# Kernel optimization log

Hardware: AMD Instinct MI355X
Metric: run time of the kernel (lower is better)

## Reference

```python
import jax, jax.numpy as jnp
import numpy as np

B, S, T, V, E, H, D, A = 16, 128, 128, 32000, 512, 512, 512, 512
ENC = 2 * H  # bidirectional encoder output dim
NEG = -1e9


def _w(key, shape, scale=0.05):
    return scale * jax.random.normal(key, shape, dtype=jnp.float32)


def setup_inputs() -> dict:
    key = jax.random.key(0)
    ks = jax.random.split(key, 26)
    src = jax.random.randint(ks[0], (B, S), 1, V)
    tgt = jax.random.randint(ks[1], (B, T), 1, V)
    src_lens = jnp.full((B,), S, dtype=jnp.int32)  # full-length sequences (pack == identity)
    return dict(
        src=src, src_lens=src_lens, tgt=tgt,
        enc_embed=_w(ks[2], (V, E)).at[0].set(0.0),   # padding_idx=0
        Wih_f=_w(ks[3], (4 * H, E)), Whh_f=_w(ks[4], (4 * H, H)),
        bih_f=_w(ks[5], (4 * H,)), bhh_f=_w(ks[6], (4 * H,)),
        Wih_b=_w(ks[7], (4 * H, E)), Whh_b=_w(ks[8], (4 * H, H)),
        bih_b=_w(ks[9], (4 * H,)), bhh_b=_w(ks[10], (4 * H,)),
        Wbh=_w(ks[11], (D, 2 * H)), bbh=_w(ks[12], (D,)),
        Wbc=_w(ks[13], (D, 2 * H)), bbc=_w(ks[14], (D,)),
        Wh_att=_w(ks[15], (A, ENC)), Ws_att=_w(ks[16], (A, D)), v_att=_w(ks[17], (A,)),
        dec_embed=_w(ks[18], (V, E)).at[0].set(0.0),  # padding_idx=0
        Wih_d=_w(ks[19], (4 * D, E + ENC)), Whh_d=_w(ks[20], (4 * D, D)),
        bih_d=_w(ks[21], (4 * D,)), bhh_d=_w(ks[22], (4 * D,)),
        Wfc=_w(ks[23], (V, D + ENC)), bfc=_w(ks[24], (V,)),
    )


def _lstm_cell(x, h, c, Wih, Whh, bih, bhh):
    # PyTorch gate order: i, f, g, o
    g = x @ Wih.T + h @ Whh.T + (bih + bhh)
    i, f, gg, o = jnp.split(g, 4, axis=-1)
    c = jax.nn.sigmoid(f) * c + jax.nn.sigmoid(i) * jnp.tanh(gg)
    h = jax.nn.sigmoid(o) * jnp.tanh(c)
    return h, c


def _run_lstm(xs, Wih, Whh, bih, bhh, hdim):
    # xs: [S, B, E] -> (hs [S, B, hdim], h_last, c_last)
    b = xs.shape[1]
    h0 = jnp.zeros((b, hdim), xs.dtype)

    def step(carry, x):
        h, c = carry
        h, c = _lstm_cell(x, h, c, Wih, Whh, bih, bhh)
        return (h, c), h

    (hT, cT), hs = jax.lax.scan(step, (h0, h0), xs)
    return hs, hT, cT


def reference(src, src_lens, tgt, enc_embed, Wih_f, Whh_f, bih_f, bhh_f,
              Wih_b, Whh_b, bih_b, bhh_b, Wbh, bbh, Wbc, bbc,
              Wh_att, Ws_att, v_att, dec_embed, Wih_d, Whh_d, bih_d, bhh_d,
              Wfc, bfc):
    # ---- BiLSTM encoder (src_lens == S, so packing is the identity) ----
    emb = enc_embed[src]                      # [B, S, E]
    xs = jnp.swapaxes(emb, 0, 1)              # [S, B, E]
    hs_f, hf, _ = _run_lstm(xs, Wih_f, Whh_f, bih_f, bhh_f, H)
    hs_b, hb, _ = _run_lstm(xs[::-1], Wih_b, Whh_b, bih_b, bhh_b, H)
    hs_b = hs_b[::-1]
    enc_out = jnp.swapaxes(jnp.concatenate([hs_f, hs_b], axis=-1), 0, 1)  # [B, S, 2H]

    # ---- bridge (num_layers = 1) ----
    h_cat = jnp.concatenate([hf, hb], axis=-1)  # [B, 2H]
    h0 = jnp.tanh(h_cat @ Wbh.T + bbh)          # [B, D]
    c_cat = jnp.concatenate([hf, hb], axis=-1)
    c0 = jnp.tanh(c_cat @ Wbc.T + bbc)

    mask = jnp.arange(S)[None, :] < src_lens[:, None]  # [B, S]
    enc_proj = jnp.einsum('bse,ae->bsa', enc_out, Wh_att)  # W_h(enc_out), hoisted

    # ---- decoder loop, teacher_forcing = 1.0 ----
    def dec_step(carry, inp_t):
        h, c = carry
        # Bahdanau attention on top-layer hidden state
        score = jnp.einsum('bsa,a->bs', jnp.tanh(enc_proj + (h @ Ws_att.T)[:, None, :]), v_att)
        score = jnp.where(mask, score, NEG)
        attn = jax.nn.softmax(score, axis=-1)
        ctx = jnp.einsum('bs,bse->be', attn, enc_out)       # [B, 2H]
        x = jnp.concatenate([dec_embed[inp_t], ctx], axis=-1)  # [B, E+2H]
        h, c = _lstm_cell(x, h, c, Wih_d, Whh_d, bih_d, bhh_d)
        logits = jnp.concatenate([h, ctx], axis=-1) @ Wfc.T + bfc  # [B, V]
        return (h, c), logits

    inps = tgt[:, :-1].T  # [T-1, B]
    _, logits = jax.lax.scan(dec_step, (h0, c0), inps)
    return jnp.swapaxes(logits, 0, 1)  # [B, T-1, V]
```

## Files before the change

kernel.cpp:

```cpp
#include <hip/hip_runtime.h>

typedef __bf16 bf16x8 __attribute__((ext_vector_type(8)));
typedef float f32x4 __attribute__((ext_vector_type(4)));
typedef unsigned short us;
typedef unsigned long long ull;

#define DEV static __device__ __forceinline__

DEV float bf2f(us u){ union { unsigned u; float f; } x; x.u = ((unsigned)u) << 16; return x.f; }
DEV us f2bf(float f){
  union { float f; unsigned u; } x; x.f = f;
  unsigned r = x.u + 0x7fffu + ((x.u >> 16) & 1u);
  return (us)(r >> 16);
}
DEV unsigned pack2(us lo, us hi){ return (unsigned)lo | ((unsigned)hi << 16); }
DEV float sigm(float x){ return 1.0f / (1.0f + expf(-x)); }
DEV float tanh_fast(float x){ float e = __expf(2.0f * x); return 1.0f - 2.0f / (e + 1.0f); }
DEV void unpk2(unsigned u, float& a, float& b){ a = bf2f((us)u); b = bf2f((us)(u >> 16)); }

DEV unsigned ld4v(const unsigned* p){ return __hip_atomic_load(p, __ATOMIC_RELAXED, __HIP_MEMORY_SCOPE_AGENT); }
DEV ull ld8v(const void* p){ return __hip_atomic_load((const ull*)p, __ATOMIC_RELAXED, __HIP_MEMORY_SCOPE_AGENT); }
DEV void st4v(unsigned* p, unsigned v){ __hip_atomic_store(p, v, __ATOMIC_RELAXED, __HIP_MEMORY_SCOPE_AGENT); }

DEV void gridbar3(unsigned* arr, unsigned ep){
  __syncthreads();
  if (threadIdx.x == 0)
    __hip_atomic_store(arr + (size_t)blockIdx.x * 16, ep, __ATOMIC_RELEASE, __HIP_MEMORY_SCOPE_AGENT);
  if (threadIdx.x < 128){
    while (__hip_atomic_load(arr + (size_t)threadIdx.x * 16, __ATOMIC_RELAXED, __HIP_MEMORY_SCOPE_AGENT) < ep)
      __builtin_amdgcn_s_sleep(4);
  }
  __syncthreads();
}

DEV void groupbar(unsigned* gbase, int slot, unsigned ep){
  __syncthreads();
  if (threadIdx.x == 0)
    __hip_atomic_store(gbase + slot * 16, ep, __ATOMIC_RELEASE, __HIP_MEMORY_SCOPE_AGENT);
  if (threadIdx.x < 8){
    while (__hip_atomic_load(gbase + threadIdx.x * 16, __ATOMIC_RELAXED, __HIP_MEMORY_SCOPE_AGENT) < ep)
      __builtin_amdgcn_s_sleep(2);
  }
  __syncthreads();
}

__global__ void k_f2bf(const float4* __restrict__ in, uint2* __restrict__ out, long n4){
  long stride = (long)gridDim.x * blockDim.x;
  for (long i = (long)blockIdx.x * blockDim.x + threadIdx.x; i < n4; i += stride){
    float4 v = in[i];
    uint2 o; o.x = pack2(f2bf(v.x), f2bf(v.y)); o.y = pack2(f2bf(v.z), f2bf(v.w));
    out[i] = o;
  }
}

__global__ void k_bias3(const float* a0, const float* b0, float* o0,
                        const float* a1, const float* b1, float* o1,
                        const float* a2, const float* b2, float* o2){
  int i = blockIdx.x * 256 + threadIdx.x;
  o0[i] = a0[i] + b0[i];
  o1[i] = a1[i] + b1[i];
  o2[i] = a2[i] + b2[i];
}

__global__ void k_embed(const int* __restrict__ tok, const float* __restrict__ table,
                        us* __restrict__ out){
  int r = blockIdx.x;
  int b = r & 15, pos = r >> 4;
  int idx = tok[b * 128 + pos];
  float4 v = ((const float4*)(table + (size_t)idx * 512))[threadIdx.x];
  uint2 o; o.x = pack2(f2bf(v.x), f2bf(v.y)); o.y = pack2(f2bf(v.z), f2bf(v.w));
  ((uint2*)(out + (size_t)r * 512))[threadIdx.x] = o;
}

template<int MODE>
__global__ __launch_bounds__(256)
void gemm_bt(const us* __restrict__ A, int lda,
             const us* __restrict__ B, int ldb,
             const float* __restrict__ bias,
             void* __restrict__ Cv, int ldc, int K, int mvalid)
{
  __shared__ __align__(16) us As[128 * 64];
  __shared__ __align__(16) us Bs[128 * 64];
  const int tid  = threadIdx.x;
  const int lane = tid & 63, wid = tid >> 6;
  const int wm = (wid >> 1) * 64, wn = (wid & 1) * 64;
  const us* Ab = A + (size_t)blockIdx.y * 128 * lda;
  const us* Bb = B + (size_t)blockIdx.x * 128 * ldb;

  f32x4 acc[4][4] = {};
  bf16x8 ga[4], gb[4];

  #pragma unroll
  for (int r = 0; r < 4; r++){
    int c = tid + r * 256;
    ga[r] = *(const bf16x8*)(Ab + (size_t)(c >> 3) * lda + (c & 7) * 8);
    gb[r] = *(const bf16x8*)(Bb + (size_t)(c >> 3) * ldb + (c & 7) * 8);
  }
  const int nt = K >> 6;
  for (int t = 0; t < nt; t++){
    #pragma unroll
    for (int r = 0; r < 4; r++){
      int c = tid + r * 256;
      int slot = ((c >> 3) * 8 + ((c & 7) ^ ((c >> 3) & 7))) * 8;
      *(bf16x8*)(As + slot) = ga[r];
      *(bf16x8*)(Bs + slot) = gb[r];
    }
    __syncthreads();
    if (t + 1 < nt){
      int k0 = (t + 1) * 64;
      #pragma unroll
      for (int r = 0; r < 4; r++){
        int c = tid + r * 256;
        ga[r] = *(const bf16x8*)(Ab + (size_t)(c >> 3) * lda + k0 + (c & 7) * 8);
        gb[r] = *(const bf16x8*)(Bb + (size_t)(c >> 3) * ldb + k0 + (c & 7) * 8);
      }
    }
    #pragma unroll
    for (int kk = 0; kk < 2; kk++){
      bf16x8 av[4], bv[4];
      #pragma unroll
      for (int i = 0; i < 4; i++){
        int ra = wm + i * 16 + (lane & 15);
        int ua = (kk * 4 + (lane >> 4)) ^ (ra & 7);
        av[i] = *(const bf16x8*)(As + (ra * 8 + ua) * 8);
        int rb = wn + i * 16 + (lane & 15);
        int ub = (kk * 4 + (lane >> 4)) ^ (rb & 7);
        bv[i] = *(const bf16x8*)(Bs + (rb * 8 + ub) * 8);
      }
      #pragma unroll
      for (int i = 0; i < 4; i++)
        #pragma unroll
        for (int j = 0; j < 4; j++)
          acc[i][j] = __builtin_amdgcn_mfma_f32_16x16x32_bf16(av[i], bv[j], acc[i][j], 0, 0, 0);
    }
    if (t + 1 < nt) __syncthreads();
  }

  const int cb = lane & 15, rb4 = (lane >> 4) * 4;
  #pragma unroll
  for (int i = 0; i < 4; i++){
    #pragma unroll
    for (int j = 0; j < 4; j++){
      #pragma unroll
      for (int r = 0; r < 4; r++){
        int row = blockIdx.y * 128 + wm + i * 16 + rb4 + r;
        int col = blockIdx.x * 128 + wn + j * 16 + cb;
        float v = acc[i][j][r];
        if (bias) v += bias[col];
        if (MODE == 0) ((float*)Cv)[(size_t)row * ldc + col] = v;
        else           ((us*)Cv)[(size_t)row * ldc + col] = f2bf(v);
      }
    }
  }
}

__global__ __launch_bounds__(256)
void enc_persist4(const float* __restrict__ gin_f, const float* __restrict__ gin_b,
                  const us* __restrict__ whhf_bf, const us* __restrict__ whhb_bf,
                  us* __restrict__ enc_out_bf,
                  unsigned* __restrict__ arr)
{
  __shared__ __align__(16) us Wt[2][1024][8];
  __shared__ __align__(16) us Hrow[2][16][520];
  __shared__ __align__(16) f32x4 P[2][4][64];
  __shared__ float gl[2][16][17];
  __shared__ float hvout[2][16][4];

  const int bx = blockIdx.x, tid = threadIdx.x;
  const int lane = tid & 63, wv = tid >> 6;

  for (int d = 0; d < 2; d++){
    const us* srcw = d ? whhb_bf : whhf_bf;
    for (int u = tid; u < 1024; u += 256){
      int ks = u >> 6, ch = (u >> 4) & 3, v = u & 15;
      int n = (v & 3) * 512 + bx * 4 + (v >> 2);
      *(bf16x8*)Wt[d][u] = *(const bf16x8*)(srcw + (size_t)n * 512 + ks * 32 + ch * 8);
    }
  }

  float creg = 0.0f;
  const int cd = (tid >> 6) & 1, cb = tid & 15, cj = (tid >> 4) & 3;

  for (int t = 0; t < 128; t++){
    if (t == 0){
      #pragma unroll
      for (int r = 0; r < 8; r++){
        int u = tid + r * 256;
        int d = u >> 10, b = (u >> 6) & 15, s16 = u & 63;
        *(ull*)&Hrow[d][b][s16 * 8]     = 0ull;
        *(ull*)&Hrow[d][b][s16 * 8 + 4] = 0ull;
      }
    } else {
      #pragma unroll
      for (int r = 0; r < 8; r++){
        int u = tid + r * 256;
        int d = u >> 10, b = (u >> 6) & 15, s16 = u & 63;
        int sp = d ? (128 - t) : (t - 1);
        const us* s = enc_out_bf + ((size_t)b * 128 + sp) * 1024 + d * 512 + s16 * 8;
        ull lo = ld8v(s), hi = ld8v(s + 4);
        *(ull*)&Hrow[d][b][s16 * 8]     = lo;
        *(ull*)&Hrow[d][b][s16 * 8 + 4] = hi;
      }
    }
    __syncthreads();
    #pragma unroll
    for (int d = 0; d < 2; d++){
      f32x4 acc = {};
      #pragma unroll
      for (int m = 0; m < 4; m++){
        int ks = wv * 4 + m;
        int ch = lane >> 4, b = lane & 15;
        acc = __builtin_amdgcn_mfma_f32_16x16x32_bf16(*(const bf16x8*)&Hrow[d][b][ks * 32 + ch * 8],
                                                      *(const bf16x8*)Wt[d][(ks * 4 + ch) * 16 + b],
                                                      acc, 0, 0, 0);
      }
      P[d][wv][lane] = acc;
    }
    __syncthreads();
    if (wv < 2){
      int d = wv;
      f32x4 sum = (P[d][0][lane] + P[d][1][lane]) + (P[d][2][lane] + P[d][3][lane]);
      int v = lane & 15;
      int n = (v & 3) * 512 + bx * 4 + (v >> 2);
      int s_in = d ? (127 - t) : t;
      const float* gg = (d ? gin_b : gin_f) + (size_t)s_in * 16 * 2048 + n;
      #pragma unroll
      for (int r = 0; r < 4; r++){
        int b = (lane >> 4) * 4 + r;
        gl[d][v][b] = sum[r] + gg[(size_t)b * 2048];
      }
    }
    __syncthreads();
    if (tid < 128){
      float ig = sigm (gl[cd][cj * 4 + 0][cb]);
      float fg = sigm (gl[cd][cj * 4 + 1][cb]);
      float g2 = tanhf(gl[cd][cj * 4 + 2][cb]);
      float og = sigm (gl[cd][cj * 4 + 3][cb]);
      float cn = fg * creg + ig * g2;
      float hv = og * tanhf(cn);
      creg = cn;
      hvout[cd][cb][cj] = hv;
    }
    __syncthreads();
    if (tid < 64){
      int d = tid >> 5, rem = tid & 31, b = rem & 15, jp = rem >> 4;
      int s_in = d ? (127 - t) : t;
      st4v((unsigned*)(enc_out_bf + ((size_t)b * 128 + s_in) * 1024 + d * 512 + bx * 4 + jp * 2),
           pack2(f2bf(hvout[d][b][jp * 2]), f2bf(hvout[d][b][jp * 2 + 1])));
    }
    if (t != 127) gridbar3(arr, t + 1);
  }
}

__global__ __launch_bounds__(512)
void k_h0c0(const us* __restrict__ enc_out_bf, const float* __restrict__ Wbh, const float* __restrict__ bbh,
            const float* __restrict__ Wbc, const float* __restrict__ bbc,
            us* __restrict__ h0_bf, float* __restrict__ c_dec)
{
  __shared__ float hc[1024];
  int b = blockIdx.x >> 1, which = blockIdx.x & 1;
  int tid = threadIdx.x;
  hc[tid]       = bf2f(enc_out_bf[((size_t)b * 128 + 127) * 1024 + tid]);
  hc[512 + tid] = bf2f(enc_out_bf[((size_t)b * 128 + 0)   * 1024 + 512 + tid]);
  __syncthreads();
  const float* W = which ? Wbc : Wbh;
  float acc = (which ? bbc : bbh)[tid];
  const float* wr = W + (size_t)tid * 1024;
  for (int k = 0; k < 1024; k += 4){
    float4 w = *(const float4*)(wr + k);
    acc += w.x * hc[k] + w.y * hc[k + 1] + w.z * hc[k + 2] + w.w * hc[k + 3];
  }
  float v = tanhf(acc);
  if (which) c_dec[b * 512 + tid] = v;
  else       h0_bf[b * 512 + tid] = f2bf(v);
}

#define SMEM_BYTES 161952

__global__ __launch_bounds__(256)
void dec_fused2(const us* __restrict__ h0_bf, const float* __restrict__ c_dec0,
                const float* __restrict__ Ws_att, const float* __restrict__ v_att,
                const us* __restrict__ enc_proj_bf, const us* __restrict__ enc_out_bf,
                const int* __restrict__ src_lens, const float* __restrict__ gin_d,
                const us* __restrict__ whhd_bf, const us* __restrict__ wihd_bf,
                float* __restrict__ hs_g, float* __restrict__ esc_g,
                us* __restrict__ hctx,
                const us* __restrict__ wfc, const float* __restrict__ bfc,
                float* __restrict__ out,
                unsigned* __restrict__ arr, unsigned* __restrict__ arrG,
                unsigned* __restrict__ tdone)
{
  __shared__ __align__(16) char smem[SMEM_BYTES];
  const int tid = threadIdx.x;

  if (blockIdx.x >= 128){
    us* As = (us*)smem;
    us* Bs = (us*)(smem + 32768);
    const int lane = tid & 63, wid = tid >> 6;
    const int wm = wid * 64;
    for (int tile = blockIdx.x - 128; tile < 2000; tile += 128){
      int rt = tile / 250, ct = tile - rt * 250;
      unsigned need = (rt == 7) ? 127u : (unsigned)(16 * rt + 16);
      if (tid == 0){
        while (ld4v(tdone) < need) __builtin_amdgcn_s_sleep(8);
      }
      __syncthreads();
      const us* Ab = hctx + (size_t)rt * 256 * 1536;
      const us* Bb = wfc  + (size_t)ct * 128 * 1536;
      f32x4 acc[4][8] = {};
      bf16x8 ga[8], gb[4];
      #pragma unroll
      for (int r = 0; r < 8; r++){
        int cc = tid + r * 256;
        int row = cc >> 3, piece = cc & 7;
        bool val = (rt * 256 + row) < 2032;
        union { ull q[2]; bf16x8 v; } u;
        const us* p = Ab + (size_t)row * 1536 + piece * 8;
        u.q[0] = val ? ld8v(p) : 0ull;
        u.q[1] = val ? ld8v(p + 4) : 0ull;
        ga[r] = u.v;
      }
      #pragma unroll
      for (int r = 0; r < 4; r++){
        int cc = tid + r * 256;
        gb[r] = *(const bf16x8*)(Bb + (size_t)(cc >> 3) * 1536 + (cc & 7) * 8);
      }
      for (int tk = 0; tk < 24; tk++){
        #pragma unroll
        for (int r = 0; r < 8; r++){
          int cc = tid + r * 256;
          int slot = ((cc >> 3) * 8 + ((cc & 7) ^ ((cc >> 3) & 7))) * 8;
          *(bf16x8*)(As + slot) = ga[r];
        }
        #pragma unroll
        for (int r = 0; r < 4; r++){
          int cc = tid + r * 256;
          int slot = ((cc >> 3) * 8 + ((cc & 7) ^ ((cc >> 3) & 7))) * 8;
          *(bf16x8*)(Bs + slot) = gb[r];
        }
        __syncthreads();
        if (tk + 1 < 24){
          int k0 = (tk + 1) * 64;
          #pragma unroll
          for (int r = 0; r < 8; r++){
            int cc = tid + r * 256;
            int row = cc >> 3, piece = cc & 7;
            bool val = (rt * 256 + row) < 2032;
            union { ull q[2]; bf16x8 v; } u;
            const us* p = Ab + (size_t)row * 1536 + k0 + piece * 8;
            u.q[0] = val ? ld8v(p) : 0ull;
            u.q[1] = val ? ld8v(p + 4) : 0ull;
            ga[r] = u.v;
          }
          #pragma unroll
          for (int r = 0; r < 4; r++){
            int cc = tid + r * 256;
            gb[r] = *(const bf16x8*)(Bb + (size_t)(cc >> 3) * 1536 + k0 + (cc & 7) * 8);
          }
        }
        #pragma unroll
        for (int kk = 0; kk < 2; kk++){
          bf16x8 av[4], bv[8];
          #pragma unroll
          for (int i = 0; i < 4; i++){
            int ra = wm + i * 16 + (lane & 15);
            int ua = (kk * 4 + (lane >> 4)) ^ (ra & 7);
            av[i] = *(const bf16x8*)(As + (ra * 8 + ua) * 8);
          }
          #pragma unroll
          for (int j = 0; j < 8; j++){
            int rb = j * 16 + (lane & 15);
            int ub = (kk * 4 + (lane >> 4)) ^ (rb & 7);
            bv[j] = *(const bf16x8*)(Bs + (rb * 8 + ub) * 8);
          }
          #pragma unroll
          for (int i = 0; i < 4; i++)
            #pragma unroll
            for (int j = 0; j < 8; j++)
              acc[i][j] = __builtin_amdgcn_mfma_f32_16x16x32_bf16(av[i], bv[j], acc[i][j], 0, 0, 0);
        }
        if (tk + 1 < 24) __syncthreads();
      }
      const int cbl = lane & 15, rb4 = (lane >> 4) * 4;
      #pragma unroll
      for (int i = 0; i < 4; i++){
        #pragma unroll
        for (int j = 0; j < 8; j++){
          #pragma unroll
          for (int r = 0; r < 4; r++){
            int row = rt * 256 + wm + i * 16 + rb4 + r;
            int col = ct * 128 + j * 16 + cbl;
            if (row < 2032){
              float v = acc[i][j][r] + bfc[col];
              int tt = row >> 4, b = row & 15;
              out[((size_t)b * 127 + tt) * 32000 + col] = v;
            }
          }
        }
      }
    }
    return;
  }

  us (*Wh)[8]      = (us(*)[8])(smem);
  us (*Wc)[8]      = (us(*)[8])(smem + 16384);
  us (*Ws64)[520]  = (us(*)[520])(smem + 49152);
  us (*Xrow)[1032] = (us(*)[1032])(smem + 115712);
  f32x4 (*P)[64]   = (f32x4(*)[64])(smem + 148736);
  float (*g1l)[17] = (float(*)[17])(smem + 152832);
  float (*gl)[17]  = (float(*)[17])(smem + 153920);
  float* vl        = (float*)(smem + 155008);
  float (*hsp)[64] = (float(*)[64])(smem + 157056);
  float* hs_b      = (float*)(smem + 158080);
  float* att       = (float*)(smem + 160128);
  float (*cred)[128] = (float(*)[128])(smem + 160640);
  float* sred      = (float*)(smem + 161664);
  float (*hvs)[4]  = (float(*)[4])(smem + 161696);

  const int bx = blockIdx.x;
  const int lane = tid & 63, wv = tid >> 6;
  const int bB = bx & 15, sQ = bx >> 4;
  unsigned* gbase = arrG + bB * 128;

  for (int u = tid; u < 1024; u += 256){
    int ks = u >> 6, ch = (u >> 4) & 3, v = u & 15;
    int n = (v & 3) * 512 + bx * 4 + (v >> 2);
    *(bf16x8*)Wh[u] = *(const bf16x8*)(whhd_bf + (size_t)n * 512 + ks * 32 + ch * 8);
  }
  for (int u = tid; u < 2048; u += 256){
    int ks = u >> 6, ch = (u >> 4) & 3, v = u & 15;
    int n = (v & 3) * 512 + bx * 4 + (v >> 2);
    *(bf16x8*)Wc[u] = *(const bf16x8*)(wihd_bf + (size_t)n * 1536 + 512 + ks * 32 + ch * 8);
  }
  for (int u = tid; u < 32768; u += 256){
    int a = u >> 9, k = u & 511;
    Ws64[a][k] = f2bf(Ws_att[(size_t)(sQ * 64 + a) * 512 + k]);
  }
  for (int u = tid; u < 512; u += 256) vl[u] = v_att[u];
  const int slen = src_lens[bB];

  float creg = 0.0f;
  if (tid < 64) creg = c_dec0[(tid & 15) * 512 + bx * 4 + (tid >> 4)];

  for (int t = 0; t < 127; t++){
    const us* hsrc = t ? (hctx + (size_t)(t - 1) * 16 * 1536) : h0_bf;
    const int hstride = t ? 1536 : 512;

    #pragma unroll
    for (int r = 0; r < 4; r++){
      int u = tid + r * 256;
      int b = u >> 6, s16 = u & 63;
      const us* s = hsrc + (size_t)b * hstride + s16 * 8;
      ull lo = ld8v(s), hi = ld8v(s + 4);
      *(ull*)&Xrow[b][s16 * 8]     = lo;
      *(ull*)&Xrow[b][s16 * 8 + 4] = hi;
    }
    __syncthreads();
    {
      f32x4 acc = {};
      #pragma unroll
      for (int m = 0; m < 4; m++){
        int ks = wv * 4 + m;
        int ch = lane >> 4, b = lane & 15;
        acc = __builtin_amdgcn_mfma_f32_16x16x32_bf16(*(const bf16x8*)&Xrow[b][ks * 32 + ch * 8],
                                                      *(const bf16x8*)Wh[(ks * 4 + ch) * 16 + b],
                                                      acc, 0, 0, 0);
      }
      P[wv][lane] = acc;
    }
    {
      const us* wr = Ws64[lane] + wv * 128;
      const us* xr = Xrow[bB] + wv * 128;
      float s = 0.f;
      #pragma unroll
      for (int k = 0; k < 128; k += 8){
        bf16x8 xv = *(const bf16x8*)(xr + k);
        bf16x8 wv8 = *(const bf16x8*)(wr + k);
        #pragma unroll
        for (int e = 0; e < 8; e++) s += (float)xv[e] * (float)wv8[e];
      }
      hsp[wv][lane] = s;
    }
    __syncthreads();
    if (wv == 0){
      f32x4 sum = (P[0][lane] + P[1][lane]) + (P[2][lane] + P[3][lane]);
      int v = lane & 15;
      int n = (v & 3) * 512 + bx * 4 + (v >> 2);
      #pragma unroll
      for (int r = 0; r < 4; r++){
        int b = (lane >> 4) * 4 + r;
        g1l[v][b] = sum[r] + gin_d[((size_t)t * 16 + b) * 2048 + n];
      }
    }
    if (tid < 64){
      float v = hsp[0][tid] + hsp[1][tid] + hsp[2][tid] + hsp[3][tid];
      st4v((unsigned*)&hs_g[bB * 512 + sQ * 64 + tid], __float_as_uint(v));
    }

    groupbar(gbase, sQ, 2 * t + 1);

    {
      ull v = ld8v(&hs_g[bB * 512 + tid * 2]);
      *(ull*)&hs_b[tid * 2] = v;
    }
    __syncthreads();
    {
      int si = tid >> 4, part = tid & 15;
      const us* er = enc_proj_bf + ((size_t)bB * 128 + sQ * 16 + si) * 512 + part * 32;
      const float* hb = hs_b + part * 32;
      const float* vp = vl + part * 32;
      float sv = 0.f;
      #pragma unroll
      for (int a = 0; a < 32; a += 8){
        uint4 u4 = *(const uint4*)(er + a);
        float e0,e1,e2,e3,e4,e5,e6,e7;
        unpk2(u4.x,e0,e1); unpk2(u4.y,e2,e3); unpk2(u4.z,e4,e5); unpk2(u4.w,e6,e7);
        sv += vp[a+0]*tanh_fast(e0+hb[a+0]) + vp[a+1]*tanh_fast(e1+hb[a+1])
            + vp[a+2]*tanh_fast(e2+hb[a+2]) + vp[a+3]*tanh_fast(e3+hb[a+3])
            + vp[a+4]*tanh_fast(e4+hb[a+4]) + vp[a+5]*tanh_fast(e5+hb[a+5])
            + vp[a+6]*tanh_fast(e6+hb[a+6]) + vp[a+7]*tanh_fast(e7+hb[a+7]);
      }
      sv += __shfl_xor(sv, 1);
      sv += __shfl_xor(sv, 2);
      sv += __shfl_xor(sv, 4);
      sv += __shfl_xor(sv, 8);
      if (part == 0){
        int s = sQ * 16 + si;
        float e = (s < slen) ? __expf(sv) : 0.f;
        st4v((unsigned*)&esc_g[bB * 128 + s], __float_as_uint(e));
      }
    }

    groupbar(gbase, sQ, 2 * t + 2);

    {
      float e = 0.f;
      if (tid < 128) e = __uint_as_float(ld4v((unsigned*)&esc_g[bB * 128 + tid]));
      if (tid < 128) att[tid] = e;
      float ss = e;
      #pragma unroll
      for (int o = 32; o; o >>= 1) ss += __shfl_xor(ss, o);
      if (lane == 0) sred[wv] = ss;
    }
    __syncthreads();
    {
      int kk = tid & 127, half = tid >> 7;
      const float* ab = att + half * 64;
      const us* er = enc_out_bf + ((size_t)(bB * 128 + half * 64)) * 1024 + sQ * 128 + kk;
      float s = 0.f;
      #pragma unroll 8
      for (int s2 = 0; s2 < 64; s2++)
        s += ab[s2] * bf2f(er[(size_t)s2 * 1024]);
      cred[half][kk] = s;
    }
    __syncthreads();
    if (tid < 64){
      float inv = 1.0f / (sred[0] + sred[1] + sred[2] + sred[3]);
      int kk2 = tid * 2;
      float c0 = (cred[0][kk2]     + cred[1][kk2])     * inv;
      float c1 = (cred[0][kk2 + 1] + cred[1][kk2 + 1]) * inv;
      st4v((unsigned*)(hctx + ((size_t)t * 16 + bB) * 1536 + 512 + sQ * 128 + kk2),
           pack2(f2bf(c0), f2bf(c1)));
    }

    gridbar3(arr, 2 * t + 1);

    #pragma unroll
    for (int r = 0; r < 8; r++){
      int u = tid + r * 256;
      int b = u >> 7, s16 = u & 127;
      const us* s = hctx + ((size_t)t * 16 + b) * 1536 + 512 + s16 * 8;
      ull lo = ld8v(s), hi = ld8v(s + 4);
      *(ull*)&Xrow[b][s16 * 8]     = lo;
      *(ull*)&Xrow[b][s16 * 8 + 4] = hi;
    }
    __syncthreads();
    {
      f32x4 acc = {};
      #pragma unroll
      for (int m = 0; m < 8; m++){
        int ks = wv * 8 + m;
        int ch = lane >> 4, b = lane & 15;
        acc = __builtin_amdgcn_mfma_f32_16x16x32_bf16(*(const bf16x8*)&Xrow[b][ks * 32 + ch * 8],
                                                      *(const bf16x8*)Wc[(ks * 4 + ch) * 16 + b],
                                                      acc, 0, 0, 0);
      }
      P[wv][lane] = acc;
    }
    __syncthreads();
    if (wv == 0){
      f32x4 sum = (P[0][lane] + P[1][lane]) + (P[2][lane] + P[3][lane]);
      int v = lane & 15;
      #pragma unroll
      for (int r = 0; r < 4; r++){
        int b = (lane >> 4) * 4 + r;
        gl[v][b] = sum[r] + g1l[v][b];
      }
    }
    __syncthreads();
    if (tid < 64){
      int b2 = tid & 15, joff = tid >> 4;
      float ig = sigm (gl[joff * 4 + 0][b2]);
      float fg = sigm (gl[joff * 4 + 1][b2]);
      float g2 = tanhf(gl[joff * 4 + 2][b2]);
      float og = sigm (gl[joff * 4 + 3][b2]);
      float cn = fg * creg + ig * g2;
      float hv = og * tanhf(cn);
      creg = cn;
      hvs[b2][joff] = hv;
    }
    __syncthreads();
    if (tid < 32){
      int b = tid & 15, jp = tid >> 4;
      st4v((unsigned*)(hctx + ((size_t)t * 16 + b) * 1536 + bx * 4 + jp * 2),
           pack2(f2bf(hvs[b][jp * 2]), f2bf(hvs[b][jp * 2 + 1])));
    }
    gridbar3(arr, 2 * t + 2);
    if (bx == 0 && tid == 0)
      __hip_atomic_store(tdone, (unsigned)(t + 1), __ATOMIC_RELEASE, __HIP_MEMORY_SCOPE_AGENT);
  }
}

extern "C" void kernel_launch(void* const* d_in, const int* in_sizes, int n_in,
                              void* d_out, int out_size, void* d_ws, size_t ws_size,
                              hipStream_t stream)
{
  const int*   src       = (const int*)d_in[0];
  const int*   src_lens  = (const int*)d_in[1];
  const int*   tgt       = (const int*)d_in[2];
  const float* enc_embed = (const float*)d_in[3];
  const float* Wih_f = (const float*)d_in[4];
  const float* Whh_f = (const float*)d_in[5];
  const float* bih_f = (const float*)d_in[6];
  const float* bhh_f = (const float*)d_in[7];
  const float* Wih_b = (const float*)d_in[8];
  const float* Whh_b = (const float*)d_in[9];
  const float* bih_b = (const float*)d_in[10];
  const float* bhh_b = (const float*)d_in[11];
  const float* Wbh = (const float*)d_in[12];
  const float* bbh = (const float*)d_in[13];
  const float* Wbc = (const float*)d_in[14];
  const float* bbc = (const float*)d_in[15];
  const float* Wh_att = (const float*)d_in[16];
  const float* Ws_att = (const float*)d_in[17];
  const float* v_att  = (const float*)d_in[18];
  const float* dec_embed = (const float*)d_in[19];
  const float* Wih_d = (const float*)d_in[20];
  const float* Whh_d = (const float*)d_in[21];
  const float* bih_d = (const float*)d_in[22];
  const float* bhh_d = (const float*)d_in[23];
  const float* Wfc = (const float*)d_in[24];
  const float* bfc = (const float*)d_in[25];
  float* out = (float*)d_out;

  char* base = (char*)d_ws;
  size_t off = 0;
  auto take = [&](size_t bytes) -> char* {
    char* p = base + off;
    off += (bytes + 255) & ~(size_t)255;
    return p;
  };
  us* wfc_bf    = (us*)take((size_t)32000 * 1536 * 2);
  us* emb_e     = (us*)take((size_t)2048 * 512 * 2);
  us* emb_d     = (us*)take((size_t)2048 * 512 * 2);
  us* wihf_bf   = (us*)take((size_t)2048 * 512 * 2);
  us* wihb_bf   = (us*)take((size_t)2048 * 512 * 2);
  us* wihd_bf   = (us*)take((size_t)2048 * 1536 * 2);
  us* whhf_bf   = (us*)take((size_t)2048 * 512 * 2);
  us* whhb_bf   = (us*)take((size_t)2048 * 512 * 2);
  us* whhd_bf   = (us*)take((size_t)2048 * 512 * 2);
  us* whatt_bf  = (us*)take((size_t)512 * 1024 * 2);
  float* gin_f    = (float*)take((size_t)2048 * 2048 * 4);
  float* gin_b    = (float*)take((size_t)2048 * 2048 * 4);
  float* gin_d    = (float*)take((size_t)2048 * 2048 * 4);
  us* enc_out_bf  = (us*)take((size_t)2048 * 1024 * 2);
  us* enc_proj_bf = (us*)take((size_t)2048 * 512 * 2);
  us* hctx        = (us*)take((size_t)2048 * 1536 * 2);
  us* h0_bf       = (us*)take((size_t)16 * 512 * 2);
  float* c_dec    = (float*)take((size_t)16 * 512 * 4);
  float* hs_g     = (float*)take((size_t)16 * 512 * 4);
  float* esc_g    = (float*)take((size_t)16 * 128 * 4);
  float* bias_f = (float*)take(2048 * 4);
  float* bias_b = (float*)take(2048 * 4);
  float* bias_d = (float*)take(2048 * 4);
  unsigned* arrE  = (unsigned*)take(128 * 16 * 4);
  unsigned* arrD  = (unsigned*)take(128 * 16 * 4);
  unsigned* arrG  = (unsigned*)take(16 * 8 * 16 * 4);
  unsigned* tdone = (unsigned*)take(256);

  hipMemsetAsync(emb_d, 0, (size_t)2048 * 512 * 2, stream);
  hipMemsetAsync(hctx, 0, (size_t)2048 * 1536 * 2, stream);
  hipMemsetAsync(arrE, 0, (128 * 16 + 128 * 16 + 16 * 8 * 16) * 4 + 256, stream);

  k_f2bf<<<4096, 256, 0, stream>>>((const float4*)Wfc,   (uint2*)wfc_bf,   (long)32000 * 1536 / 4);
  k_f2bf<<<512,  256, 0, stream>>>((const float4*)Wih_f, (uint2*)wihf_bf,  (long)2048 * 512 / 4);
  k_f2bf<<<512,  256, 0, stream>>>((const float4*)Wih_b, (uint2*)wihb_bf,  (long)2048 * 512 / 4);
  k_f2bf<<<1024, 256, 0, stream>>>((const float4*)Wih_d, (uint2*)wihd_bf,  (long)2048 * 1536 / 4);
  k_f2bf<<<512,  256, 0, stream>>>((const float4*)Whh_f, (uint2*)whhf_bf,  (long)2048 * 512 / 4);
  k_f2bf<<<512,  256, 0, stream>>>((const float4*)Whh_b, (uint2*)whhb_bf,  (long)2048 * 512 / 4);
  k_f2bf<<<512,  256, 0, stream>>>((const float4*)Whh_d, (uint2*)whhd_bf,  (long)2048 * 512 / 4);
  k_f2bf<<<512,  256, 0, stream>>>((const float4*)Wh_att,(uint2*)whatt_bf, (long)512 * 1024 / 4);
  k_bias3<<<8, 256, 0, stream>>>(bih_f, bhh_f, bias_f, bih_b, bhh_b, bias_b, bih_d, bhh_d, bias_d);

  k_embed<<<2048, 128, 0, stream>>>(src, enc_embed, emb_e);
  k_embed<<<2032, 128, 0, stream>>>(tgt, dec_embed, emb_d);

  gemm_bt<0><<<dim3(16, 16), 256, 0, stream>>>(emb_e, 512, wihf_bf, 512,  bias_f, gin_f, 2048, 512, 4096);
  gemm_bt<0><<<dim3(16, 16), 256, 0, stream>>>(emb_e, 512, wihb_bf, 512,  bias_b, gin_b, 2048, 512, 4096);
  gemm_bt<0><<<dim3(16, 16), 256, 0, stream>>>(emb_d, 512, wihd_bf, 1536, bias_d, gin_d, 2048, 512, 4096);

  enc_persist4<<<128, 256, 0, stream>>>(gin_f, gin_b, whhf_bf, whhb_bf, enc_out_bf, arrE);

  k_h0c0<<<32, 512, 0, stream>>>(enc_out_bf, Wbh, bbh, Wbc, bbc, h0_bf, c_dec);

  gemm_bt<2><<<dim3(4, 16), 256, 0, stream>>>(enc_out_bf, 1024, whatt_bf, 1024, nullptr, enc_proj_bf, 512, 1024, 4096);

  dec_fused2<<<256, 256, 0, stream>>>(h0_bf, c_dec, Ws_att, v_att, enc_proj_bf, enc_out_bf, src_lens,
                                      gin_d, whhd_bf, wihd_bf, hs_g, esc_g, hctx,
                                      wfc_bf, bfc, out, arrD, arrG, tdone);
}
```

Measured before the change: 3.866 ms.

## Compute partial attention scores per block to drop one group barrier per step

Each block of the 8-block group for a batch row now computes partial attention scores over its own 64-wide slice of the attention dimension for all 128 source positions, using its locally held hidden projection. This removes the exchange of the full hidden projection and one of the two group barriers per decoder step. The partial scores are published to global memory and summed after a single barrier. The change also switches the output-projection weight loads to nontemporal loads. It trades extra global score traffic, 1024 floats per batch row per step, for one fewer cross-block synchronisation on the serial decoder path.

```diff
diff --git a/kernel.cpp b/kernel.cpp
--- a/kernel.cpp
+++ b/kernel.cpp
@@ -275,15 +275,15 @@
   else       h0_bf[b * 512 + tid] = f2bf(v);
 }
 
-#define SMEM_BYTES 161952
+#define SMEM_BYTES 162464
 
 __global__ __launch_bounds__(256)
-void dec_fused2(const us* __restrict__ h0_bf, const float* __restrict__ c_dec0,
+void dec_fused3(const us* __restrict__ h0_bf, const float* __restrict__ c_dec0,
                 const float* __restrict__ Ws_att, const float* __restrict__ v_att,
                 const us* __restrict__ enc_proj_bf, const us* __restrict__ enc_out_bf,
                 const int* __restrict__ src_lens, const float* __restrict__ gin_d,
                 const us* __restrict__ whhd_bf, const us* __restrict__ wihd_bf,
-                float* __restrict__ hs_g, float* __restrict__ esc_g,
+                float* __restrict__ pscore_g,
                 us* __restrict__ hctx,
                 const us* __restrict__ wfc, const float* __restrict__ bfc,
                 float* __restrict__ out,
@@ -323,7 +323,7 @@
       #pragma unroll
       for (int r = 0; r < 4; r++){
         int cc = tid + r * 256;
-        gb[r] = *(const bf16x8*)(Bb + (size_t)(cc >> 3) * 1536 + (cc & 7) * 8);
+        gb[r] = __builtin_nontemporal_load((const bf16x8*)(Bb + (size_t)(cc >> 3) * 1536 + (cc & 7) * 8));
       }
       for (int tk = 0; tk < 24; tk++){
         #pragma unroll
@@ -355,7 +355,7 @@
           #pragma unroll
           for (int r = 0; r < 4; r++){
             int cc = tid + r * 256;
-            gb[r] = *(const bf16x8*)(Bb + (size_t)(cc >> 3) * 1536 + k0 + (cc & 7) * 8);
+            gb[r] = __builtin_nontemporal_load((const bf16x8*)(Bb + (size_t)(cc >> 3) * 1536 + k0 + (cc & 7) * 8));
           }
         }
         #pragma unroll
@@ -409,13 +409,14 @@
   f32x4 (*P)[64]   = (f32x4(*)[64])(smem + 148736);
   float (*g1l)[17] = (float(*)[17])(smem + 152832);
   float (*gl)[17]  = (float(*)[17])(smem + 153920);
-  float* vl        = (float*)(smem + 155008);
-  float (*hsp)[64] = (float(*)[64])(smem + 157056);
-  float* hs_b      = (float*)(smem + 158080);
-  float* att       = (float*)(smem + 160128);
-  float (*cred)[128] = (float(*)[128])(smem + 160640);
-  float* sred      = (float*)(smem + 161664);
-  float (*hvs)[4]  = (float(*)[4])(smem + 161696);
+  float* vl64      = (float*)(smem + 155008);
+  float (*hsp)[64] = (float(*)[64])(smem + 155264);
+  float* hs_own    = (float*)(smem + 156288);
+  float (*pall)[128] = (float(*)[128])(smem + 156544);
+  float* att       = (float*)(smem + 160640);
+  float (*cred)[128] = (float(*)[128])(smem + 161152);
+  float* sred      = (float*)(smem + 162176);
+  float (*hvs)[4]  = (float(*)[4])(smem + 162208);
 
   const int bx = blockIdx.x;
   const int lane = tid & 63, wv = tid >> 6;
@@ -436,7 +437,7 @@
     int a = u >> 9, k = u & 511;
     Ws64[a][k] = f2bf(Ws_att[(size_t)(sQ * 64 + a) * 512 + k]);
   }
-  for (int u = tid; u < 512; u += 256) vl[u] = v_att[u];
+  if (tid < 64) vl64[tid] = v_att[sQ * 64 + tid];
   const int slen = src_lens[bB];
 
   float creg = 0.0f;
@@ -492,23 +493,13 @@
         g1l[v][b] = sum[r] + gin_d[((size_t)t * 16 + b) * 2048 + n];
       }
     }
-    if (tid < 64){
-      float v = hsp[0][tid] + hsp[1][tid] + hsp[2][tid] + hsp[3][tid];
-      st4v((unsigned*)&hs_g[bB * 512 + sQ * 64 + tid], __float_as_uint(v));
-    }
-
-    groupbar(gbase, sQ, 2 * t + 1);
-
+    if (tid < 64) hs_own[tid] = hsp[0][tid] + hsp[1][tid] + hsp[2][tid] + hsp[3][tid];
+    __syncthreads();
     {
-      ull v = ld8v(&hs_g[bB * 512 + tid * 2]);
-      *(ull*)&hs_b[tid * 2] = v;
-    }
-    __syncthreads();
-    {
-      int si = tid >> 4, part = tid & 15;
-      const us* er = enc_proj_bf + ((size_t)bB * 128 + sQ * 16 + si) * 512 + part * 32;
-      const float* hb = hs_b + part * 32;
-      const float* vp = vl + part * 32;
+      int s = tid >> 1, half = tid & 1;
+      const us* er = enc_proj_bf + ((size_t)bB * 128 + s) * 512 + sQ * 64 + half * 32;
+      const float* hb = hs_own + half * 32;
+      const float* vp = vl64 + half * 32;
       float sv = 0.f;
       #pragma unroll
       for (int a = 0; a < 32; a += 8){
@@ -521,22 +512,23 @@
             + vp[a+6]*tanh_fast(e6+hb[a+6]) + vp[a+7]*tanh_fast(e7+hb[a+7]);
       }
       sv += __shfl_xor(sv, 1);
-      sv += __shfl_xor(sv, 2);
-      sv += __shfl_xor(sv, 4);
-      sv += __shfl_xor(sv, 8);
-      if (part == 0){
-        int s = sQ * 16 + si;
-        float e = (s < slen) ? __expf(sv) : 0.f;
-        st4v((unsigned*)&esc_g[bB * 128 + s], __float_as_uint(e));
-      }
-    }
-
-    groupbar(gbase, sQ, 2 * t + 2);
-
+      if (half == 0)
+        st4v((unsigned*)&pscore_g[(size_t)bB * 1024 + sQ * 128 + s], __float_as_uint(sv));
+    }
+
+    groupbar(gbase, sQ, t + 1);
+
+    for (int u = tid; u < 1024; u += 256)
+      (&pall[0][0])[u] = __uint_as_float(ld4v((unsigned*)&pscore_g[(size_t)bB * 1024 + u]));
+    __syncthreads();
     {
       float e = 0.f;
-      if (tid < 128) e = __uint_as_float(ld4v((unsigned*)&esc_g[bB * 128 + tid]));
-      if (tid < 128) att[tid] = e;
+      if (tid < 128){
+        float sc = ((pall[0][tid] + pall[1][tid]) + (pall[2][tid] + pall[3][tid]))
+                 + ((pall[4][tid] + pall[5][tid]) + (pall[6][tid] + pall[7][tid]));
+        e = (tid < slen) ? __expf(sc) : 0.f;
+        att[tid] = e;
+      }
       float ss = e;
       #pragma unroll
       for (int o = 32; o; o >>= 1) ss += __shfl_xor(ss, o);
@@ -678,8 +670,7 @@
   us* hctx        = (us*)take((size_t)2048 * 1536 * 2);
   us* h0_bf       = (us*)take((size_t)16 * 512 * 2);
   float* c_dec    = (float*)take((size_t)16 * 512 * 4);
-  float* hs_g     = (float*)take((size_t)16 * 512 * 4);
-  float* esc_g    = (float*)take((size_t)16 * 128 * 4);
+  float* pscore_g = (float*)take((size_t)16 * 1024 * 4);
   float* bias_f = (float*)take(2048 * 4);
   float* bias_b = (float*)take(2048 * 4);
   float* bias_d = (float*)take(2048 * 4);
@@ -715,7 +706,7 @@
 
   gemm_bt<2><<<dim3(4, 16), 256, 0, stream>>>(enc_out_bf, 1024, whatt_bf, 1024, nullptr, enc_proj_bf, 512, 1024, 4096);
 
-  dec_fused2<<<256, 256, 0, stream>>>(h0_bf, c_dec, Ws_att, v_att, enc_proj_bf, enc_out_bf, src_lens,
-                                      gin_d, whhd_bf, wihd_bf, hs_g, esc_g, hctx,
+  dec_fused3<<<256, 256, 0, stream>>>(h0_bf, c_dec, Ws_att, v_att, enc_proj_bf, enc_out_bf, src_lens,
+                                      gin_d, whhd_bf, wihd_bf, pscore_g, hctx,
                                       wfc_bf, bfc, out, arrD, arrG, tdone);
 }
```

Result: faster. 3.678 ms (-4.9%).
